# Kernel tuning notes

Measured on AMD Instinct MI355X. Metric: run time of the kernel, lower is better.

The kernel has to match this reference:

```python
import jax, jax.numpy as jnp
import numpy as np

N, C, H, W = 8, 192, 112, 112
TEMPERATURE = 0.1


def setup_inputs() -> dict:
    key = jax.random.key(0)
    k1, k2 = jax.random.split(key)
    features = jax.random.normal(k1, (N, C, H, W), dtype=jnp.float32)
    # Raw per-pixel directions in {-1, 0, 1}; clip the neighbor coordinate into
    # bounds and recompute the direction so EVERY neighbor is valid. The torch
    # module's broadcasting (labels[:, i, j] vs an (N, M) gather) only works when
    # all N neighbors are valid at each pixel, so this matches its assumptions.
    raw = jax.random.randint(k2, (N, 2, H, W), -1, 2)
    ii = jnp.arange(H)[None, :, None]
    jj = jnp.arange(W)[None, None, :]
    d0 = jnp.clip(ii + raw[:, 0], 0, H - 1) - ii
    d1 = jnp.clip(jj + raw[:, 1], 0, W - 1) - jj
    directions = jnp.stack([d0, d1], axis=1).astype(jnp.int32)
    # Single-class labels: the original loss is -inf whenever any mask entry is 0
    # (log of exactly 0), so a finite, comparable baseline needs matching labels.
    labels = jnp.zeros((N, H, W), dtype=jnp.int32)
    return {"features": features, "labels": labels, "directions": directions}


def reference(features, labels, directions):
    # F.normalize(features, dim=1): x / max(||x||_2, eps)
    norm = jnp.linalg.norm(features, axis=1, keepdims=True)
    fn = features / jnp.maximum(norm, 1e-12)

    ii = jnp.arange(H)[None, :, None]
    jj = jnp.arange(W)[None, None, :]
    ni = ii + directions[:, 0]  # (N, H, W), in-bounds by construction
    nj = jj + directions[:, 1]  # (N, H, W)

    # Torch: features[:, :, neighbor_i, neighbor_j] gathers the M(==N) neighbor
    # coordinates across ALL batch elements -> (N, C, N, H, W) = [n, c, m, i, j]
    gathered = fn[:, :, ni, nj]
    # logits[n, m, i, j] = <fn[n, :, i, j], fn[n, :, ni[m,i,j], nj[m,i,j]]> / T
    logits = jnp.einsum('ncij,ncmij->nmij', fn, gathered) / TEMPERATURE

    # mask[n, m, i, j] = (labels[m, i, j] == labels[n, ni[m,i,j], nj[m,i,j]])
    # (torch broadcasts labels[:, i, j] along the first axis of the (N, M) gather)
    labels_g = labels[:, ni, nj]  # (N, N, H, W) = [n, m, i, j]
    mask = (labels[None, :, :, :] == labels_g).astype(fn.dtype)

    exp_l = jnp.exp(logits) * mask
    denom = jnp.sum(exp_l, axis=1, keepdims=True)  # sum over m
    # sum_{i,j} mean_{n,m}(.) / (H*W) == global mean over (n, m, i, j)
    loss = (-jnp.log(exp_l / (denom + 1e-6))).mean()
    return loss
```

## Files before the change

### kernel.cpp

```cpp
#include <hip/hip_runtime.h>
#include <math.h>


namespace {
constexpr int N_ = 8, C_ = 192, H_ = 112, W_ = 112;
constexpr int HW = H_ * W_;
constexpr int TH = 2;
constexpr int TROWS = TH + 2;
constexpr int TWID = W_ + 2;
constexpr int TILE_E = TROWS * TWID;
constexpr int NT = 256;
constexpr int NPX = TH * W_;
constexpr int EXTRA = TILE_E - NT;
constexpr int KCH = 4;
constexpr int NCHUNK = C_ / KCH;
constexpr float INV_T = 10.0f;
constexpr double TOTAL = (double)N_ * N_ * H_ * W_;
}

__device__ __forceinline__ float sel3(int d, float a, float b, float c) {
    float r = (d < 0) ? a : b;
    return (d > 0) ? c : r;
}

extern "C" __global__ void __launch_bounds__(NT, 2)
dcl_main(const float* __restrict__ feat,
         const int* __restrict__ labels,
         const int* __restrict__ dirs,
         double* __restrict__ acc)
{
    __shared__ float2 tiles[2][2][TILE_E];
    __shared__ float ssbuf[TILE_E];
    __shared__ float red[NT / 64];

    const int tid = threadIdx.x;
    const int n   = blockIdx.y;
    const int gy0 = blockIdx.x * TH;

    int gofs0, gofs1 = 0;
    {
        int r = tid / TWID, col = tid - r * TWID;
        gofs0 = min(max(gy0 + r - 1, 0), H_ - 1) * W_ + min(max(col - 1, 0), W_ - 1);
        if (tid < EXTRA) {
            int t2 = tid + NT;
            r = t2 / TWID; col = t2 - r * TWID;
            gofs1 = min(max(gy0 + r - 1, 0), H_ - 1) * W_ + min(max(col - 1, 0), W_ - 1);
        }
    }

    const bool is_px = (tid < NPX);
    const int ty = tid / W_;
    const int tx = tid - ty * W_;
    const int gi = gy0 + ty;
    const int gj = tx;
    const int ci = (ty + 1) * TWID + (tx + 1);

    const float* __restrict__ plane = feat + (size_t)n * C_ * HW;

    float ss0 = 0.0f, ss1 = 0.0f;

    {
        float v0 = plane[gofs0], v1 = plane[HW + gofs0];
        float v2 = plane[2 * HW + gofs0], v3 = plane[3 * HW + gofs0];
        ss0 += v0 * v0 + v1 * v1 + v2 * v2 + v3 * v3;
        tiles[0][0][tid] = make_float2(v0, v1);
        tiles[0][1][tid] = make_float2(v2, v3);
        if (tid < EXTRA) {
            float u0 = plane[gofs1], u1 = plane[HW + gofs1];
            float u2 = plane[2 * HW + gofs1], u3 = plane[3 * HW + gofs1];
            ss1 += u0 * u0 + u1 * u1 + u2 * u2 + u3 * u3;
            tiles[0][0][tid + NT] = make_float2(u0, u1);
            tiles[0][1][tid + NT] = make_float2(u2, u3);
        }
    }
    __syncthreads();

    float s[9];
    #pragma unroll
    for (int d = 0; d < 9; ++d) s[d] = 0.0f;

    for (int t = 0; t < NCHUNK; ++t) {
        float pv0[KCH], pv1[KCH];
        const bool more = (t + 1 < NCHUNK);
        if (more) {
            const float* p = plane + (size_t)(t + 1) * KCH * HW;
            #pragma unroll
            for (int k = 0; k < KCH; ++k) pv0[k] = p[(size_t)k * HW + gofs0];
            if (tid < EXTRA) {
                #pragma unroll
                for (int k = 0; k < KCH; ++k) pv1[k] = p[(size_t)k * HW + gofs1];
            }
        }

        if (is_px) {
            #pragma unroll
            for (int g = 0; g < 2; ++g) {
                const float2* __restrict__ cp = tiles[t & 1][g];
                float2 fc  = cp[ci];
                float2 n00 = cp[ci - TWID - 1];
                float2 n01 = cp[ci - TWID];
                float2 n02 = cp[ci - TWID + 1];
                float2 n10 = cp[ci - 1];
                float2 n12 = cp[ci + 1];
                float2 n20 = cp[ci + TWID - 1];
                float2 n21 = cp[ci + TWID];
                float2 n22 = cp[ci + TWID + 1];
                s[0] = fmaf(fc.x, n00.x, s[0]); s[0] = fmaf(fc.y, n00.y, s[0]);
                s[1] = fmaf(fc.x, n01.x, s[1]); s[1] = fmaf(fc.y, n01.y, s[1]);
                s[2] = fmaf(fc.x, n02.x, s[2]); s[2] = fmaf(fc.y, n02.y, s[2]);
                s[3] = fmaf(fc.x, n10.x, s[3]); s[3] = fmaf(fc.y, n10.y, s[3]);
                s[4] = fmaf(fc.x, fc.x,  s[4]); s[4] = fmaf(fc.y, fc.y,  s[4]);
                s[5] = fmaf(fc.x, n12.x, s[5]); s[5] = fmaf(fc.y, n12.y, s[5]);
                s[6] = fmaf(fc.x, n20.x, s[6]); s[6] = fmaf(fc.y, n20.y, s[6]);
                s[7] = fmaf(fc.x, n21.x, s[7]); s[7] = fmaf(fc.y, n21.y, s[7]);
                s[8] = fmaf(fc.x, n22.x, s[8]); s[8] = fmaf(fc.y, n22.y, s[8]);
            }
        }

        if (more) {
            float2* nxt0 = tiles[(t + 1) & 1][0];
            float2* nxt1 = tiles[(t + 1) & 1][1];
            ss0 += pv0[0]*pv0[0] + pv0[1]*pv0[1] + pv0[2]*pv0[2] + pv0[3]*pv0[3];
            nxt0[tid] = make_float2(pv0[0], pv0[1]);
            nxt1[tid] = make_float2(pv0[2], pv0[3]);
            if (tid < EXTRA) {
                ss1 += pv1[0]*pv1[0] + pv1[1]*pv1[1] + pv1[2]*pv1[2] + pv1[3]*pv1[3];
                nxt0[tid + NT] = make_float2(pv1[0], pv1[1]);
                nxt1[tid + NT] = make_float2(pv1[2], pv1[3]);
            }
            __syncthreads();
        }
    }

    __syncthreads();
    ssbuf[tid] = 1.0f / fmaxf(sqrtf(ss0), 1e-12f);
    if (tid < EXTRA)
        ssbuf[tid + NT] = 1.0f / fmaxf(sqrtf(ss1), 1e-12f);
    __syncthreads();

    float lp = 0.0f;
    if (is_px) {
        const float invc = ssbuf[ci] * INV_T;
        const float l00 = s[0] * invc * ssbuf[ci - TWID - 1];
        const float l01 = s[1] * invc * ssbuf[ci - TWID];
        const float l02 = s[2] * invc * ssbuf[ci - TWID + 1];
        const float l10 = s[3] * invc * ssbuf[ci - 1];
        const float l11 = s[4] * invc * ssbuf[ci];
        const float l12 = s[5] * invc * ssbuf[ci + 1];
        const float l20 = s[6] * invc * ssbuf[ci + TWID - 1];
        const float l21 = s[7] * invc * ssbuf[ci + TWID];
        const float l22 = s[8] * invc * ssbuf[ci + TWID + 1];

        const int pix = gi * W_ + gj;
        float denom = 0.f, sumlog = 0.f;
        #pragma unroll
        for (int m = 0; m < N_; ++m) {
            int d0 = dirs[((m * 2 + 0) * H_ + gi) * W_ + gj];
            int d1 = dirs[((m * 2 + 1) * H_ + gi) * W_ + gj];
            float q0 = sel3(d1, l00, l01, l02);
            float q1 = sel3(d1, l10, l11, l12);
            float q2 = sel3(d1, l20, l21, l22);
            float lm = sel3(d0, q0, q1, q2);
            int labm = labels[m * HW + pix];
            int labn = labels[n * HW + (gi + d0) * W_ + (gj + d1)];
            bool msk = (labm == labn);
            float e = msk ? __expf(lm) : 0.f;
            denom += e;
            sumlog += msk ? lm : -INFINITY;
        }
        lp = 8.0f * __logf(denom + 1e-6f) - sumlog;
    }

    #pragma unroll
    for (int off = 32; off > 0; off >>= 1) lp += __shfl_down(lp, off, 64);
    const int wave = tid >> 6, lane = tid & 63;
    if (lane == 0) red[wave] = lp;
    __syncthreads();
    if (tid == 0) {
        float t = red[0] + red[1] + red[2] + red[3];
        atomicAdd(acc, (double)t);
    }
}

extern "C" __global__ void dcl_final(const double* __restrict__ acc,
                                     float* __restrict__ out)
{
    out[0] = (float)(acc[0] / TOTAL);
}

extern "C" void kernel_launch(void* const* d_in, const int* in_sizes, int n_in,
                              void* d_out, int out_size, void* d_ws, size_t ws_size,
                              hipStream_t stream) {
    const float* feat   = (const float*)d_in[0];
    const int*   labels = (const int*)d_in[1];
    const int*   dirs   = (const int*)d_in[2];
    double* acc = (double*)d_ws;
    float*  out = (float*)d_out;

    hipMemsetAsync(acc, 0, sizeof(double), stream);
    dim3 grid(H_ / TH, N_);
    dcl_main<<<grid, NT, 0, stream>>>(feat, labels, dirs, acc);
    dcl_final<<<1, 1, 0, stream>>>(acc, out);
}
```

Measured before the change: 136.7 us.

## Split row tiles into half-width blocks, widen channel chunk, use per-block partial sums

Each block now covers a 2x56 pixel tile instead of a full 2x112 row pair, with 128 threads and a launch bound allowing four blocks per CU. This doubles the grid to 896 blocks for better load balance. The channel chunk per pipeline stage grows from 4 to 8, halving the number of barriers at the cost of more registers and shared memory per stage. The single double atomic plus memset is replaced, when workspace allows, by per-block partial writes reduced by a 256-thread final kernel. The halo overhead per tile goes up with the narrower tile.

```diff
diff --git a/kernel.cpp b/kernel.cpp
--- a/kernel.cpp
+++ b/kernel.cpp
@@ -6,14 +6,17 @@
 constexpr int N_ = 8, C_ = 192, H_ = 112, W_ = 112;
 constexpr int HW = H_ * W_;
 constexpr int TH = 2;
+constexpr int WS = 56;
 constexpr int TROWS = TH + 2;
-constexpr int TWID = W_ + 2;
-constexpr int TILE_E = TROWS * TWID;
-constexpr int NT = 256;
-constexpr int NPX = TH * W_;
+constexpr int TCOLS = WS + 2;
+constexpr int TILE_E = TROWS * TCOLS;
+constexpr int NT = 128;
+constexpr int NPX = TH * WS;
 constexpr int EXTRA = TILE_E - NT;
-constexpr int KCH = 4;
+constexpr int KCH = 8;
+constexpr int GRP = KCH / 2;
 constexpr int NCHUNK = C_ / KCH;
+constexpr int NBLK = 2 * (H_ / TH) * N_;
 constexpr float INV_T = 10.0f;
 constexpr double TOTAL = (double)N_ * N_ * H_ * W_;
 }
@@ -23,54 +26,59 @@
     return (d > 0) ? c : r;
 }
 
-extern "C" __global__ void __launch_bounds__(NT, 2)
+extern "C" __global__ void __launch_bounds__(NT, 4)
 dcl_main(const float* __restrict__ feat,
          const int* __restrict__ labels,
          const int* __restrict__ dirs,
-         double* __restrict__ acc)
+         double* __restrict__ partial, int use_partial)
 {
-    __shared__ float2 tiles[2][2][TILE_E];
+    __shared__ float2 tiles[2][GRP][TILE_E];
     __shared__ float ssbuf[TILE_E];
     __shared__ float red[NT / 64];
 
     const int tid = threadIdx.x;
-    const int n   = blockIdx.y;
-    const int gy0 = blockIdx.x * TH;
+    const int gx0 = blockIdx.x * WS;
+    const int gy0 = blockIdx.y * TH;
+    const int n   = blockIdx.z;
 
     int gofs0, gofs1 = 0;
     {
-        int r = tid / TWID, col = tid - r * TWID;
-        gofs0 = min(max(gy0 + r - 1, 0), H_ - 1) * W_ + min(max(col - 1, 0), W_ - 1);
+        int r = tid / TCOLS, c = tid - r * TCOLS;
+        gofs0 = min(max(gy0 + r - 1, 0), H_ - 1) * W_ + min(max(gx0 + c - 1, 0), W_ - 1);
         if (tid < EXTRA) {
             int t2 = tid + NT;
-            r = t2 / TWID; col = t2 - r * TWID;
-            gofs1 = min(max(gy0 + r - 1, 0), H_ - 1) * W_ + min(max(col - 1, 0), W_ - 1);
+            r = t2 / TCOLS; c = t2 - r * TCOLS;
+            gofs1 = min(max(gy0 + r - 1, 0), H_ - 1) * W_ + min(max(gx0 + c - 1, 0), W_ - 1);
         }
     }
 
     const bool is_px = (tid < NPX);
-    const int ty = tid / W_;
-    const int tx = tid - ty * W_;
+    const int ty = tid / WS;
+    const int tx = tid - ty * WS;
     const int gi = gy0 + ty;
-    const int gj = tx;
-    const int ci = (ty + 1) * TWID + (tx + 1);
+    const int gj = gx0 + tx;
+    const int ci = (ty + 1) * TCOLS + (tx + 1);
 
     const float* __restrict__ plane = feat + (size_t)n * C_ * HW;
 
     float ss0 = 0.0f, ss1 = 0.0f;
 
     {
-        float v0 = plane[gofs0], v1 = plane[HW + gofs0];
-        float v2 = plane[2 * HW + gofs0], v3 = plane[3 * HW + gofs0];
-        ss0 += v0 * v0 + v1 * v1 + v2 * v2 + v3 * v3;
-        tiles[0][0][tid] = make_float2(v0, v1);
-        tiles[0][1][tid] = make_float2(v2, v3);
+        #pragma unroll
+        for (int g = 0; g < GRP; ++g) {
+            float v0 = plane[(size_t)(2 * g) * HW + gofs0];
+            float v1 = plane[(size_t)(2 * g + 1) * HW + gofs0];
+            ss0 += v0 * v0 + v1 * v1;
+            tiles[0][g][tid] = make_float2(v0, v1);
+        }
         if (tid < EXTRA) {
-            float u0 = plane[gofs1], u1 = plane[HW + gofs1];
-            float u2 = plane[2 * HW + gofs1], u3 = plane[3 * HW + gofs1];
-            ss1 += u0 * u0 + u1 * u1 + u2 * u2 + u3 * u3;
-            tiles[0][0][tid + NT] = make_float2(u0, u1);
-            tiles[0][1][tid + NT] = make_float2(u2, u3);
+            #pragma unroll
+            for (int g = 0; g < GRP; ++g) {
+                float u0 = plane[(size_t)(2 * g) * HW + gofs1];
+                float u1 = plane[(size_t)(2 * g + 1) * HW + gofs1];
+                ss1 += u0 * u0 + u1 * u1;
+                tiles[0][g][tid + NT] = make_float2(u0, u1);
+            }
         }
     }
     __syncthreads();
@@ -94,17 +102,17 @@
 
         if (is_px) {
             #pragma unroll
-            for (int g = 0; g < 2; ++g) {
+            for (int g = 0; g < GRP; ++g) {
                 const float2* __restrict__ cp = tiles[t & 1][g];
                 float2 fc  = cp[ci];
-                float2 n00 = cp[ci - TWID - 1];
-                float2 n01 = cp[ci - TWID];
-                float2 n02 = cp[ci - TWID + 1];
+                float2 n00 = cp[ci - TCOLS - 1];
+                float2 n01 = cp[ci - TCOLS];
+                float2 n02 = cp[ci - TCOLS + 1];
                 float2 n10 = cp[ci - 1];
                 float2 n12 = cp[ci + 1];
-                float2 n20 = cp[ci + TWID - 1];
-                float2 n21 = cp[ci + TWID];
-                float2 n22 = cp[ci + TWID + 1];
+                float2 n20 = cp[ci + TCOLS - 1];
+                float2 n21 = cp[ci + TCOLS];
+                float2 n22 = cp[ci + TCOLS + 1];
                 s[0] = fmaf(fc.x, n00.x, s[0]); s[0] = fmaf(fc.y, n00.y, s[0]);
                 s[1] = fmaf(fc.x, n01.x, s[1]); s[1] = fmaf(fc.y, n01.y, s[1]);
                 s[2] = fmaf(fc.x, n02.x, s[2]); s[2] = fmaf(fc.y, n02.y, s[2]);
@@ -118,15 +126,19 @@
         }
 
         if (more) {
-            float2* nxt0 = tiles[(t + 1) & 1][0];
-            float2* nxt1 = tiles[(t + 1) & 1][1];
-            ss0 += pv0[0]*pv0[0] + pv0[1]*pv0[1] + pv0[2]*pv0[2] + pv0[3]*pv0[3];
-            nxt0[tid] = make_float2(pv0[0], pv0[1]);
-            nxt1[tid] = make_float2(pv0[2], pv0[3]);
+            #pragma unroll
+            for (int g = 0; g < GRP; ++g) {
+                float v0 = pv0[2 * g], v1 = pv0[2 * g + 1];
+                ss0 += v0 * v0 + v1 * v1;
+                tiles[(t + 1) & 1][g][tid] = make_float2(v0, v1);
+            }
             if (tid < EXTRA) {
-                ss1 += pv1[0]*pv1[0] + pv1[1]*pv1[1] + pv1[2]*pv1[2] + pv1[3]*pv1[3];
-                nxt0[tid + NT] = make_float2(pv1[0], pv1[1]);
-                nxt1[tid + NT] = make_float2(pv1[2], pv1[3]);
+                #pragma unroll
+                for (int g = 0; g < GRP; ++g) {
+                    float u0 = pv1[2 * g], u1 = pv1[2 * g + 1];
+                    ss1 += u0 * u0 + u1 * u1;
+                    tiles[(t + 1) & 1][g][tid + NT] = make_float2(u0, u1);
+                }
             }
             __syncthreads();
         }
@@ -141,15 +153,15 @@
     float lp = 0.0f;
     if (is_px) {
         const float invc = ssbuf[ci] * INV_T;
-        const float l00 = s[0] * invc * ssbuf[ci - TWID - 1];
-        const float l01 = s[1] * invc * ssbuf[ci - TWID];
-        const float l02 = s[2] * invc * ssbuf[ci - TWID + 1];
+        const float l00 = s[0] * invc * ssbuf[ci - TCOLS - 1];
+        const float l01 = s[1] * invc * ssbuf[ci - TCOLS];
+        const float l02 = s[2] * invc * ssbuf[ci - TCOLS + 1];
         const float l10 = s[3] * invc * ssbuf[ci - 1];
         const float l11 = s[4] * invc * ssbuf[ci];
         const float l12 = s[5] * invc * ssbuf[ci + 1];
-        const float l20 = s[6] * invc * ssbuf[ci + TWID - 1];
-        const float l21 = s[7] * invc * ssbuf[ci + TWID];
-        const float l22 = s[8] * invc * ssbuf[ci + TWID + 1];
+        const float l20 = s[6] * invc * ssbuf[ci + TCOLS - 1];
+        const float l21 = s[7] * invc * ssbuf[ci + TCOLS];
+        const float l22 = s[8] * invc * ssbuf[ci + TCOLS + 1];
 
         const int pix = gi * W_ + gj;
         float denom = 0.f, sumlog = 0.f;
@@ -177,15 +189,26 @@
     if (lane == 0) red[wave] = lp;
     __syncthreads();
     if (tid == 0) {
-        float t = red[0] + red[1] + red[2] + red[3];
-        atomicAdd(acc, (double)t);
-    }
-}
-
-extern "C" __global__ void dcl_final(const double* __restrict__ acc,
-                                     float* __restrict__ out)
+        const int bid = (blockIdx.z * gridDim.y + blockIdx.y) * gridDim.x + blockIdx.x;
+        float t = red[0] + red[1];
+        if (use_partial) partial[bid] = (double)t;
+        else atomicAdd(partial, (double)t);
+    }
+}
+
+extern "C" __global__ void __launch_bounds__(256)
+dcl_final(const double* __restrict__ partial, float* __restrict__ out, int nblk)
 {
-    out[0] = (float)(acc[0] / TOTAL);
+    const int tid = threadIdx.x;
+    double s = 0.0;
+    for (int i = tid; i < nblk; i += 256) s += partial[i];
+    #pragma unroll
+    for (int off = 32; off > 0; off >>= 1) s += __shfl_down(s, off, 64);
+    __shared__ double red[4];
+    const int lane = tid & 63, wv = tid >> 6;
+    if (lane == 0) red[wv] = s;
+    __syncthreads();
+    if (tid == 0) out[0] = (float)((red[0] + red[1] + red[2] + red[3]) / TOTAL);
 }
 
 extern "C" void kernel_launch(void* const* d_in, const int* in_sizes, int n_in,
@@ -197,8 +220,9 @@
     double* acc = (double*)d_ws;
     float*  out = (float*)d_out;
 
-    hipMemsetAsync(acc, 0, sizeof(double), stream);
-    dim3 grid(H_ / TH, N_);
-    dcl_main<<<grid, NT, 0, stream>>>(feat, labels, dirs, acc);
-    dcl_final<<<1, 1, 0, stream>>>(acc, out);
-}
+    const int use_partial = (ws_size >= (size_t)NBLK * sizeof(double)) ? 1 : 0;
+    if (!use_partial) hipMemsetAsync(acc, 0, sizeof(double), stream);
+    dim3 grid(2, H_ / TH, N_);
+    dcl_main<<<grid, NT, 0, stream>>>(feat, labels, dirs, acc, use_partial);
+    dcl_final<<<1, 256, 0, stream>>>(acc, out, use_partial ? NBLK : 1);
+}
```

New measurement: 127.0 us. 7.1% less time.
